# Kernel optimization log

Hardware: AMD Instinct MI355X
Metric: run time of the kernel (lower is better)

Reference implementation:

```python
import jax, jax.numpy as jnp
import numpy as np

NUM_EMBEDDINGS = 1024
EMBEDDING_DIM = 256
COMMITMENT_COST = 0.25
EMA_DECAY = 0.99
EPSILON = 1e-10


def setup_inputs() -> dict:
    key = jax.random.key(0)
    k1, k2, k3 = jax.random.split(key, 3)
    z_e = jax.random.normal(k1, (32, EMBEDDING_DIM, 32, 32), dtype=jnp.float32)
    embedding = jax.random.normal(k2, (NUM_EMBEDDINGS, EMBEDDING_DIM), dtype=jnp.float32)
    ema_cluster_size = jnp.zeros((NUM_EMBEDDINGS,), dtype=jnp.float32)
    ema_w = jax.random.normal(k3, (NUM_EMBEDDINGS, EMBEDDING_DIM), dtype=jnp.float32)
    return {"z_e": z_e, "embedding": embedding,
            "ema_cluster_size": ema_cluster_size, "ema_w": ema_w}


def reference(z_e, embedding, ema_cluster_size, ema_w):
    B, C, H, W = z_e.shape
    K = embedding.shape[0]
    # [B,C,H,W] -> [B,H,W,C] -> [N,C]
    z_bhwc = jnp.transpose(z_e, (0, 2, 3, 1))
    z_flat = z_bhwc.reshape(-1, C)
    N = z_flat.shape[0]

    # squared-L2 distances: ||z||^2 + ||e||^2 - 2 z e^T  -> [N, K]
    distances = (jnp.sum(z_flat * z_flat, axis=1, keepdims=True)
                 + jnp.sum(embedding * embedding, axis=1)
                 - 2.0 * z_flat @ embedding.T)
    indices = jnp.argmin(distances, axis=1)  # [N]

    quantized = embedding[indices].reshape(z_bhwc.shape)  # [B,H,W,C]

    # EMA codebook update (training path); segment_sum replaces one-hot matmul
    counts = jax.ops.segment_sum(jnp.ones((N,), dtype=z_flat.dtype), indices,
                                 num_segments=K)
    new_cluster_size = ema_cluster_size * EMA_DECAY + (1.0 - EMA_DECAY) * counts
    dw = jax.ops.segment_sum(z_flat, indices, num_segments=K)  # [K, C]
    new_ema_w = ema_w * EMA_DECAY + (1.0 - EMA_DECAY) * dw
    n = jnp.sum(new_cluster_size)
    cluster_size = (new_cluster_size + EPSILON) / (n + K * EPSILON) * n
    new_embedding = new_ema_w / cluster_size[:, None]

    loss = COMMITMENT_COST * jnp.mean(
        (jax.lax.stop_gradient(quantized) - z_bhwc) ** 2)
    # straight-through estimator
    q_st = z_bhwc + jax.lax.stop_gradient(quantized - z_bhwc)

    avg_probs = counts / N
    perplexity = jnp.exp(-jnp.sum(avg_probs * jnp.log(avg_probs + 1e-10)))

    q_out = jnp.transpose(q_st, (0, 3, 1, 2))  # [B,C,H,W]
    token_map = indices.reshape(B, H, W)
    return (q_out, loss, perplexity, token_map,
            new_cluster_size, new_ema_w, new_embedding)
```

## Files before the change

### kernel.cpp

```cpp
#include <hip/hip_runtime.h>

#define C_DIM   256
#define HWN     1024
#define N_TOT   32768
#define NELEM   8388608
#define CHW     (C_DIM*HWN)
#define BIGF    3.4e38f
#define FLAG_CAP 8192
#define MARGIN  0.02f

typedef __attribute__((ext_vector_type(8)))  short bf16x8;
typedef __attribute__((ext_vector_type(16))) float f32x16;


__device__ inline unsigned short bf16_rne(float x) {
    unsigned int u = __float_as_uint(x);
    unsigned int r = (u + 0x7FFF + ((u >> 16) & 1)) >> 16;
    return (unsigned short)r;
}
__device__ inline float bf16_to_f(unsigned short h) {
    return __uint_as_float(((unsigned int)h) << 16);
}

__global__ __launch_bounds__(256)
void vq_eprep(const float* __restrict__ e, unsigned short* __restrict__ ebt) {
    const int t = threadIdx.x;
    const int ct = blockIdx.x;
    const int cg = blockIdx.y;
    const int u = t >> 5;
    const int row = t & 31;
    const float* src = e + (size_t)(ct*32 + row)*C_DIM + cg*64 + u*8;
    const float4 v0 = *(const float4*)(src);
    const float4 v1 = *(const float4*)(src + 4);
    const float xs[8] = {v0.x,v0.y,v0.z,v0.w,v1.x,v1.y,v1.z,v1.w};
    __align__(16) unsigned short hi[8], lo[8];
    #pragma unroll
    for (int j = 0; j < 8; j++) {
        hi[j] = bf16_rne(xs[j]);
        lo[j] = bf16_rne(xs[j] - bf16_to_f(hi[j]));
    }
    const int cs = cg*4 + (u >> 1);
    const int lpos = (u & 1)*32 + row;
    unsigned short* dhi = ebt + ((size_t)(ct*2 + 0)*16 + cs)*512 + lpos*8;
    unsigned short* dlo = ebt + ((size_t)(ct*2 + 1)*16 + cs)*512 + lpos*8;
    *(uint4*)dhi = *(const uint4*)hi;
    *(uint4*)dlo = *(const uint4*)lo;
}

__global__ void vq_enorm(const float* __restrict__ e, float* __restrict__ enorm) {
    const int t = threadIdx.x;
    const int w = t >> 6;
    const int lane = t & 63;
    const int k = blockIdx.x * 4 + w;
    const float4 v = *(const float4*)(e + (size_t)k * C_DIM + lane * 4);
    float s = fmaf(v.x, v.x, fmaf(v.y, v.y, fmaf(v.z, v.z, v.w * v.w)));
    #pragma unroll
    for (int off = 32; off > 0; off >>= 1) s += __shfl_down(s, off, 64);
    if (lane == 0) enorm[k] = s;
}

__global__ __launch_bounds__(256)
void vq_zprep(const float* __restrict__ z, unsigned short* __restrict__ zbt) {
    const int t = threadIdx.x;
    const int rt = blockIdx.x;
    const int cg = blockIdx.y;
    const int u = t >> 5;
    const int row = t & 31;
    const int n = rt*32 + row;
    const int b = n >> 10, p = n & 1023;
    const float* zb = z + (size_t)b*CHW + p;
    const int c0 = cg*64 + u*8;
    float xs[8];
    #pragma unroll
    for (int j = 0; j < 8; j++) xs[j] = zb[(size_t)(c0 + j)*HWN];
    __align__(16) unsigned short hi[8], lo[8];
    #pragma unroll
    for (int j = 0; j < 8; j++) {
        hi[j] = bf16_rne(xs[j]);
        lo[j] = bf16_rne(xs[j] - bf16_to_f(hi[j]));
    }
    const int cs = cg*4 + (u >> 1);
    const int lpos = (u & 1)*32 + row;
    unsigned short* base = zbt + (size_t)rt*16384;
    *(uint4*)(base + (0*16 + cs)*512 + lpos*8) = *(const uint4*)hi;
    *(uint4*)(base + (16   + cs)*512 + lpos*8) = *(const uint4*)lo;
}

__global__ __launch_bounds__(256, 2)
void vq_argmin_mfma(const unsigned short* __restrict__ zbt,
                    const unsigned short* __restrict__ ebt,
                    const float* __restrict__ enorm,
                    int* __restrict__ idx_arr, int* __restrict__ counts_i,
                    float* __restrict__ tokmap,
                    int* __restrict__ flag_cnt, int* __restrict__ flags) {
    __shared__ float redd[64][2];
    __shared__ float reds[64][2];
    __shared__ int   redi[64][2];

    const int t = threadIdx.x;
    const int lane = t & 63;
    const int w = t >> 6;
    const int rg = w >> 1;
    const int cg = w & 1;
    const int col = lane & 31;
    const int h = lane >> 5;
    const int n0 = blockIdx.x * 64;
    const int rt = (n0 >> 5) + rg;

    bf16x8 Ahi[16], Alo[16];
    const unsigned short* abase = zbt + (size_t)rt * 16384;
    #pragma unroll
    for (int cs = 0; cs < 16; cs++) {
        Ahi[cs] = *(const bf16x8*)(abase + (0*16 + cs)*512 + lane*8);
        Alo[cs] = *(const bf16x8*)(abase + (16   + cs)*512 + lane*8);
    }

    float bestd[16], secondd[16];
    int   besti[16];
    #pragma unroll
    for (int r = 0; r < 16; r++) { bestd[r] = BIGF; secondd[r] = BIGF; besti[r] = 0x7fffffff; }

    for (int kc = 0; kc < 16; kc++) {
        f32x16 acc = {0,0,0,0,0,0,0,0,0,0,0,0,0,0,0,0};
        const unsigned short* bh_base = ebt + ((size_t)((kc*2 + cg)*2 + 0)*16)*512 + lane*8;
        const unsigned short* bl_base = bh_base + (size_t)16*512;
        #pragma unroll
        for (int cs = 0; cs < 16; cs++) {
            const bf16x8 bh = *(const bf16x8*)(bh_base + (size_t)cs*512);
            const bf16x8 bl = *(const bf16x8*)(bl_base + (size_t)cs*512);
            acc = __builtin_amdgcn_mfma_f32_32x32x16_bf16(Ahi[cs], bh, acc, 0, 0, 0);
            acc = __builtin_amdgcn_mfma_f32_32x32x16_bf16(Ahi[cs], bl, acc, 0, 0, 0);
            acc = __builtin_amdgcn_mfma_f32_32x32x16_bf16(Alo[cs], bh, acc, 0, 0, 0);
        }
        const int code = kc*64 + cg*32 + col;
        const float en = enorm[code];
        #pragma unroll
        for (int r = 0; r < 16; r++) {
            const float d = fmaf(-2.0f, acc[r], en);
            if (d < bestd[r]) { secondd[r] = bestd[r]; bestd[r] = d; besti[r] = code; }
            else if (d < secondd[r]) secondd[r] = d;
        }
    }

    #pragma unroll
    for (int m = 1; m < 32; m <<= 1) {
        #pragma unroll
        for (int r = 0; r < 16; r++) {
            const float od = __shfl_xor(bestd[r],   m, 64);
            const int   oi = __shfl_xor(besti[r],   m, 64);
            const float os = __shfl_xor(secondd[r], m, 64);
            const bool take = (od < bestd[r]) || (od == bestd[r] && oi < besti[r]);
            const float ns = take ? fminf(bestd[r], os) : fminf(secondd[r], od);
            if (take) { bestd[r] = od; besti[r] = oi; }
            secondd[r] = ns;
        }
    }
    __syncthreads();
    if (col == 0) {
        #pragma unroll
        for (int r = 0; r < 16; r++) {
            const int row = (r & 3) + 8*(r >> 2) + 4*h;
            redd[rg*32 + row][cg] = bestd[r];
            redi[rg*32 + row][cg] = besti[r];
            reds[rg*32 + row][cg] = secondd[r];
        }
    }
    __syncthreads();
    if (t < 64) {
        const float d0 = redd[t][0], d1 = redd[t][1];
        const int   i0 = redi[t][0], i1 = redi[t][1];
        const float s0 = reds[t][0], s1 = reds[t][1];
        const bool take = (d1 < d0) || (d1 == d0 && i1 < i0);
        const float bd = take ? d1 : d0;
        const int   bi = take ? i1 : i0;
        const float sd = take ? fminf(d0, s1) : fminf(s0, d1);
        const int n = n0 + t;
        idx_arr[n] = bi;
        tokmap[n] = (float)bi;
        atomicAdd(&counts_i[bi], 1);
        if (sd - bd < MARGIN) {
            const int pos = atomicAdd(flag_cnt, 1);
            if (pos < FLAG_CAP) flags[pos] = n;
        }
    }
}

__global__ __launch_bounds__(256)
void vq_fix(const float* __restrict__ z, const float* __restrict__ e,
            const float* __restrict__ enorm,
            const int* __restrict__ flag_cnt, const int* __restrict__ flags,
            int* __restrict__ idx_arr, int* __restrict__ counts_i,
            float* __restrict__ tokmap) {
    __shared__ float zrow[256];
    __shared__ float rd[256];
    __shared__ int   ri[256];
    const int t = threadIdx.x;
    int cnt = *flag_cnt;
    if (cnt > FLAG_CAP) cnt = FLAG_CAP;
    for (int fi = blockIdx.x; fi < cnt; fi += (int)gridDim.x) {
        const int n = flags[fi];
        const int b = n >> 10, p = n & 1023;
        __syncthreads();
        zrow[t] = z[(size_t)b*CHW + (size_t)t*HWN + p];
        __syncthreads();
        float bd = BIGF; int bi = 0;
        for (int q = 0; q < 4; q++) {
            const int k = t*4 + q;
            const float* er = e + (size_t)k*C_DIM;
            float acc = 0.0f;
            for (int c = 0; c < C_DIM; c += 4) {
                const float4 ev = *(const float4*)(er + c);
                acc = fmaf(ev.x, zrow[c],   acc);
                acc = fmaf(ev.y, zrow[c+1], acc);
                acc = fmaf(ev.z, zrow[c+2], acc);
                acc = fmaf(ev.w, zrow[c+3], acc);
            }
            const float d = fmaf(-2.0f, acc, enorm[k]);
            if (d < bd) { bd = d; bi = k; }
        }
        rd[t] = bd; ri[t] = bi;
        __syncthreads();
        for (int s = 128; s > 0; s >>= 1) {
            if (t < s) {
                const float d2 = rd[t+s]; const int i2 = ri[t+s];
                if (d2 < rd[t] || (d2 == rd[t] && i2 < ri[t])) { rd[t] = d2; ri[t] = i2; }
            }
            __syncthreads();
        }
        if (t == 0) {
            const int old = idx_arr[n];
            if (ri[0] != old) {
                idx_arr[n] = ri[0];
                tokmap[n] = (float)ri[0];
                atomicAdd(&counts_i[old], -1);
                atomicAdd(&counts_i[ri[0]], 1);
            }
        }
        __syncthreads();
    }
}

__global__ void vq_scan_small(const int* __restrict__ counts_i,
                              const float* __restrict__ ema_cs,
                              float* __restrict__ out_perp,
                              float* __restrict__ out_ncs,
                              float* __restrict__ csize,
                              int* __restrict__ base, int* __restrict__ offs) {
    __shared__ float sf[1024];
    __shared__ int si[1024];
    const int t = threadIdx.x;
    const int ci = counts_i[t];
    const float cnt = (float)ci;
    const float ncs = ema_cs[t] * 0.99f + 0.01f * cnt;
    out_ncs[t] = ncs;

    sf[t] = ncs;
    __syncthreads();
    for (int s = 512; s > 0; s >>= 1) { if (t < s) sf[t] += sf[t + s]; __syncthreads(); }
    const float n_total = sf[0];
    __syncthreads();

    csize[t] = (ncs + 1e-10f) / (n_total + 1024.0f * 1e-10f) * n_total;

    const float pr = cnt * (1.0f / 32768.0f);
    sf[t] = pr * logf(pr + 1e-10f);
    __syncthreads();
    for (int s = 512; s > 0; s >>= 1) { if (t < s) sf[t] += sf[t + s]; __syncthreads(); }
    if (t == 0) out_perp[0] = expf(-sf[0]);

    si[t] = ci;
    __syncthreads();
    for (int d = 1; d < 1024; d <<= 1) {
        const int x = si[t];
        const int y = (t >= d) ? si[t - d] : 0;
        __syncthreads();
        si[t] = x + y;
        __syncthreads();
    }
    const int excl = si[t] - ci;
    base[t] = excl;
    offs[t] = excl;
}

__global__ __launch_bounds__(256)
void vq_scatter(const int* __restrict__ idx_arr, int* __restrict__ offs,
                int* __restrict__ order) {
    const int n = blockIdx.x * 256 + threadIdx.x;
    const int idx = idx_arr[n];
    const int pos = atomicAdd(&offs[idx], 1);
    order[pos] = n;
}

__global__ __launch_bounds__(256)
void vq_dw(const unsigned short* __restrict__ zbt, const int* __restrict__ order,
           const int* __restrict__ base, const int* __restrict__ counts_i,
           float* __restrict__ dw) {
    __shared__ int sord[1024];
    __shared__ float red[4][256];
    const int k = blockIdx.x;
    const int t = threadIdx.x;
    const int w = t >> 6;
    const int l = t & 63;
    const int plane = l >> 5;
    const int cs = (l >> 1) & 15;
    const int hh = l & 1;
    const int start = base[k];
    const int cnt = counts_i[k];
    const size_t loff = (size_t)(plane*16 + cs)*512 + hh*256;

    float acc[8] = {0,0,0,0,0,0,0,0};

    for (int s0 = 0; s0 < cnt; s0 += 1024) {
        const int m = min(1024, cnt - s0);
        __syncthreads();
        for (int i = t; i < m; i += 256) sord[i] = order[start + s0 + i];
        __syncthreads();
        const int mm = m & ~31;
        for (int g0 = w*8; g0 < mm; g0 += 32) {
            uint4 v[8];
            #pragma unroll
            for (int r = 0; r < 8; r++) {
                const int n = sord[g0 + r];
                const int rt = n >> 5, row = n & 31;
                v[r] = *(const uint4*)(zbt + (size_t)rt*16384 + loff + row*8);
            }
            #pragma unroll
            for (int r = 0; r < 8; r++) {
                const unsigned short* u = (const unsigned short*)&v[r];
                #pragma unroll
                for (int j = 0; j < 8; j++) acc[j] += bf16_to_f(u[j]);
            }
        }
        for (int i = mm + w; i < m; i += 4) {
            const int n = sord[i];
            const int rt = n >> 5, row = n & 31;
            const uint4 v = *(const uint4*)(zbt + (size_t)rt*16384 + loff + row*8);
            const unsigned short* u = (const unsigned short*)&v;
            #pragma unroll
            for (int j = 0; j < 8; j++) acc[j] += bf16_to_f(u[j]);
        }
    }

    #pragma unroll
    for (int j = 0; j < 8; j++) acc[j] += __shfl_xor(acc[j], 32, 64);
    if (l < 32) {
        #pragma unroll
        for (int j = 0; j < 8; j++) red[w][cs*16 + hh*8 + j] = acc[j];
    }
    __syncthreads();
    dw[(size_t)k*C_DIM + t] = red[0][t] + red[1][t] + red[2][t] + red[3][t];
}

__global__ __launch_bounds__(256)
void vq_combine(const float* __restrict__ z, const float* __restrict__ e,
                const int* __restrict__ idx_arr,
                float* __restrict__ loss_acc,
                float* __restrict__ qout) {
    const int t = threadIdx.x;
    const int n = blockIdx.x * 256 + t;
    const int csplit = blockIdx.y;
    const int b = n >> 10, p = n & 1023;
    const int idx = idx_arr[n];

    const float* zrow = z + (size_t)b*CHW + p;
    float* qrow = qout + (size_t)b*CHW + p;
    const float* erow = e + (size_t)idx*C_DIM;

    float lsum = 0.0f;
    for (int cc = 0; cc < 64; cc += 16) {
        const int cb = csplit*64 + cc;
        float ev[16];
        #pragma unroll
        for (int q4 = 0; q4 < 4; q4++) {
            const float4 v = *(const float4*)(erow + cb + q4*4);
            ev[q4*4+0] = v.x; ev[q4*4+1] = v.y; ev[q4*4+2] = v.z; ev[q4*4+3] = v.w;
        }
        #pragma unroll
        for (int j = 0; j < 16; j++) {
            const float zv = zrow[(size_t)(cb + j) * HWN];
            qrow[(size_t)(cb + j) * HWN] = ev[j];
            const float df = ev[j] - zv;
            lsum = fmaf(df, df, lsum);
        }
    }
    #pragma unroll
    for (int off = 32; off > 0; off >>= 1) lsum += __shfl_down(lsum, off, 64);
    __shared__ float ls[4];
    if ((t & 63) == 0) ls[t >> 6] = lsum;
    __syncthreads();
    if (t == 0) atomicAdd(loss_acc, ls[0] + ls[1] + ls[2] + ls[3]);
}

__global__ __launch_bounds__(256)
void vq_finalize_big(const float* __restrict__ ema_w, const float* __restrict__ dw,
                     const float* __restrict__ csize, const float* __restrict__ loss_acc,
                     float* __restrict__ out_ema_w, float* __restrict__ out_emb,
                     float* __restrict__ out_loss) {
    const int i4 = blockIdx.x * 256 + threadIdx.x;
    const int k = i4 >> 6;
    const float4 w = ((const float4*)ema_w)[i4];
    const float4 d = ((const float4*)dw)[i4];
    float4 nw;
    nw.x = fmaf(w.x, 0.99f, 0.01f * d.x);
    nw.y = fmaf(w.y, 0.99f, 0.01f * d.y);
    nw.z = fmaf(w.z, 0.99f, 0.01f * d.z);
    nw.w = fmaf(w.w, 0.99f, 0.01f * d.w);
    ((float4*)out_ema_w)[i4] = nw;
    const float cs = csize[k];
    float4 ne;
    ne.x = nw.x / cs; ne.y = nw.y / cs; ne.z = nw.z / cs; ne.w = nw.w / cs;
    ((float4*)out_emb)[i4] = ne;
    if (i4 == 0) out_loss[0] = 0.25f * loss_acc[0] * (1.0f / (float)NELEM);
}

extern "C" void kernel_launch(void* const* d_in, const int* in_sizes, int n_in,
                              void* d_out, int out_size, void* d_ws, size_t ws_size,
                              hipStream_t stream) {
    const float* z      = (const float*)d_in[0];
    const float* e      = (const float*)d_in[1];
    const float* ema_cs = (const float*)d_in[2];
    const float* ema_w  = (const float*)d_in[3];
    float* out = (float*)d_out;
    float* ws  = (float*)d_ws;

    int*   idx_arr  = (int*)ws;
    int*   flag_cnt = (int*)(ws + 32768);
    int*   counts_i = (int*)(ws + 32769);
    float* loss_acc = ws + 33793;
    int*   flags    = (int*)(ws + 33794);
    float* enorm    = ws + 41986;
    float* csize    = ws + 43010;
    int*   base     = (int*)(ws + 44034);
    int*   offs     = (int*)(ws + 45058);
    int*   order    = (int*)(ws + 46082);
    unsigned short* ebt = (unsigned short*)(ws + 78852);

    unsigned short* zbt = (unsigned short*)out;
    float* dw = out + 8684546;
    float* tokmap = out + 8388610;

    hipMemsetAsync(ws + 32768, 0, 4104, stream);

    vq_eprep<<<dim3(32, 4), 256, 0, stream>>>(e, ebt);
    vq_enorm<<<256, 256, 0, stream>>>(e, enorm);
    vq_zprep<<<dim3(1024, 4), 256, 0, stream>>>(z, zbt);
    vq_argmin_mfma<<<512, 256, 0, stream>>>(zbt, ebt, enorm, idx_arr, counts_i,
                                            tokmap, flag_cnt, flags);
    vq_fix<<<64, 256, 0, stream>>>(z, e, enorm, flag_cnt, flags, idx_arr, counts_i,
                                   tokmap);
    vq_scan_small<<<1, 1024, 0, stream>>>(counts_i, ema_cs,
                                          out + 8388609, out + 8421378, csize, base, offs);
    vq_scatter<<<128, 256, 0, stream>>>(idx_arr, offs, order);
    vq_dw<<<1024, 256, 0, stream>>>(zbt, order, base, counts_i, dw);
    vq_combine<<<dim3(128, 4), 256, 0, stream>>>(z, e, idx_arr, loss_acc, out);
    vq_finalize_big<<<256, 256, 0, stream>>>(ema_w, dw, csize, loss_acc,
                                             out + 8422402, out + 8684546,
                                             out + 8388608);
}
```

Baseline: 396.0 us.

## Stage codebook tiles in LDS and split the K reduction across waves

The argmin kernel now cooperatively loads each 32-code slab of the bf16 codebook into shared memory, register-prefetching the next slab while computing the current one. Before, every wave streamed its B fragments straight from global memory. The wave pairs now split the channel dimension in half instead of splitting codes, which halves the A-fragment registers per wave. Partial MFMA accumulators are exchanged through LDS to form full dot products, and the final cross-wave argmin reduction is replaced by a per-wave direct write. The cost is two block barriers per 32-code step and twice as many outer iterations.

```diff
diff --git a/kernel.cpp b/kernel.cpp
--- a/kernel.cpp
+++ b/kernel.cpp
@@ -93,94 +93,107 @@
                     int* __restrict__ idx_arr, int* __restrict__ counts_i,
                     float* __restrict__ tokmap,
                     int* __restrict__ flag_cnt, int* __restrict__ flags) {
-    __shared__ float redd[64][2];
-    __shared__ float reds[64][2];
-    __shared__ int   redi[64][2];
+    __shared__ __align__(16) unsigned short Bslab[16384];
+    __shared__ float xbuf[2][2][8][64];
 
     const int t = threadIdx.x;
     const int lane = t & 63;
     const int w = t >> 6;
     const int rg = w >> 1;
-    const int cg = w & 1;
+    const int p  = w & 1;
     const int col = lane & 31;
     const int h = lane >> 5;
     const int n0 = blockIdx.x * 64;
     const int rt = (n0 >> 5) + rg;
 
-    bf16x8 Ahi[16], Alo[16];
+    bf16x8 Ahi[8], Alo[8];
     const unsigned short* abase = zbt + (size_t)rt * 16384;
     #pragma unroll
-    for (int cs = 0; cs < 16; cs++) {
-        Ahi[cs] = *(const bf16x8*)(abase + (0*16 + cs)*512 + lane*8);
-        Alo[cs] = *(const bf16x8*)(abase + (16   + cs)*512 + lane*8);
-    }
-
-    float bestd[16], secondd[16];
-    int   besti[16];
-    #pragma unroll
-    for (int r = 0; r < 16; r++) { bestd[r] = BIGF; secondd[r] = BIGF; besti[r] = 0x7fffffff; }
-
-    for (int kc = 0; kc < 16; kc++) {
+    for (int i = 0; i < 8; i++) {
+        Ahi[i] = *(const bf16x8*)(abase + (0*16 + p*8 + i)*512 + lane*8);
+        Alo[i] = *(const bf16x8*)(abase + (16   + p*8 + i)*512 + lane*8);
+    }
+
+    float bestd[8], secondd[8];
+    int   besti[8];
+    #pragma unroll
+    for (int j = 0; j < 8; j++) { bestd[j] = BIGF; secondd[j] = BIGF; besti[j] = 0x7fffffff; }
+
+    uint4 st[8];
+    {
+        const uint4* src = (const uint4*)ebt;
+        #pragma unroll
+        for (int i = 0; i < 8; i++) st[i] = src[i*256 + t];
+        #pragma unroll
+        for (int i = 0; i < 8; i++) ((uint4*)Bslab)[i*256 + t] = st[i];
+    }
+    __syncthreads();
+
+    for (int kc = 0; kc < 32; kc++) {
+        if (kc < 31) {
+            const uint4* src = (const uint4*)(ebt + (size_t)(kc + 1)*16384);
+            #pragma unroll
+            for (int i = 0; i < 8; i++) st[i] = src[i*256 + t];
+        }
         f32x16 acc = {0,0,0,0,0,0,0,0,0,0,0,0,0,0,0,0};
-        const unsigned short* bh_base = ebt + ((size_t)((kc*2 + cg)*2 + 0)*16)*512 + lane*8;
-        const unsigned short* bl_base = bh_base + (size_t)16*512;
-        #pragma unroll
-        for (int cs = 0; cs < 16; cs++) {
-            const bf16x8 bh = *(const bf16x8*)(bh_base + (size_t)cs*512);
-            const bf16x8 bl = *(const bf16x8*)(bl_base + (size_t)cs*512);
-            acc = __builtin_amdgcn_mfma_f32_32x32x16_bf16(Ahi[cs], bh, acc, 0, 0, 0);
-            acc = __builtin_amdgcn_mfma_f32_32x32x16_bf16(Ahi[cs], bl, acc, 0, 0, 0);
-            acc = __builtin_amdgcn_mfma_f32_32x32x16_bf16(Alo[cs], bh, acc, 0, 0, 0);
-        }
-        const int code = kc*64 + cg*32 + col;
-        const float en = enorm[code];
-        #pragma unroll
-        for (int r = 0; r < 16; r++) {
-            const float d = fmaf(-2.0f, acc[r], en);
-            if (d < bestd[r]) { secondd[r] = bestd[r]; bestd[r] = d; besti[r] = code; }
-            else if (d < secondd[r]) secondd[r] = d;
-        }
+        #pragma unroll
+        for (int i = 0; i < 8; i++) {
+            const bf16x8 bh = *(const bf16x8*)(Bslab + (0*16 + p*8 + i)*512 + lane*8);
+            const bf16x8 bl = *(const bf16x8*)(Bslab + (16   + p*8 + i)*512 + lane*8);
+            acc = __builtin_amdgcn_mfma_f32_32x32x16_bf16(Ahi[i], bh, acc, 0, 0, 0);
+            acc = __builtin_amdgcn_mfma_f32_32x32x16_bf16(Ahi[i], bl, acc, 0, 0, 0);
+            acc = __builtin_amdgcn_mfma_f32_32x32x16_bf16(Alo[i], bh, acc, 0, 0, 0);
+        }
+        if (p == 0) {
+            #pragma unroll
+            for (int j = 0; j < 8; j++) xbuf[rg][1][j][lane] = acc[8 + j];
+        } else {
+            #pragma unroll
+            for (int j = 0; j < 8; j++) xbuf[rg][0][j][lane] = acc[j];
+        }
+        __syncthreads();
+        const float en = enorm[kc*32 + col];
+        const int code = kc*32 + col;
+        #pragma unroll
+        for (int j = 0; j < 8; j++) {
+            const float mine = (p == 0) ? acc[j] : acc[8 + j];
+            const float s = mine + xbuf[rg][p][j][lane];
+            const float d = fmaf(-2.0f, s, en);
+            if (d < bestd[j]) { secondd[j] = bestd[j]; bestd[j] = d; besti[j] = code; }
+            else if (d < secondd[j]) secondd[j] = d;
+        }
+        if (kc < 31) {
+            #pragma unroll
+            for (int i = 0; i < 8; i++) ((uint4*)Bslab)[i*256 + t] = st[i];
+        }
+        __syncthreads();
     }
 
     #pragma unroll
     for (int m = 1; m < 32; m <<= 1) {
         #pragma unroll
-        for (int r = 0; r < 16; r++) {
-            const float od = __shfl_xor(bestd[r],   m, 64);
-            const int   oi = __shfl_xor(besti[r],   m, 64);
-            const float os = __shfl_xor(secondd[r], m, 64);
-            const bool take = (od < bestd[r]) || (od == bestd[r] && oi < besti[r]);
-            const float ns = take ? fminf(bestd[r], os) : fminf(secondd[r], od);
-            if (take) { bestd[r] = od; besti[r] = oi; }
-            secondd[r] = ns;
-        }
-    }
-    __syncthreads();
+        for (int j = 0; j < 8; j++) {
+            const float od = __shfl_xor(bestd[j],   m, 64);
+            const int   oi = __shfl_xor(besti[j],   m, 64);
+            const float os = __shfl_xor(secondd[j], m, 64);
+            const bool take = (od < bestd[j]) || (od == bestd[j] && oi < besti[j]);
+            const float ns = take ? fminf(bestd[j], os) : fminf(secondd[j], od);
+            if (take) { bestd[j] = od; besti[j] = oi; }
+            secondd[j] = ns;
+        }
+    }
     if (col == 0) {
         #pragma unroll
-        for (int r = 0; r < 16; r++) {
-            const int row = (r & 3) + 8*(r >> 2) + 4*h;
-            redd[rg*32 + row][cg] = bestd[r];
-            redi[rg*32 + row][cg] = besti[r];
-            reds[rg*32 + row][cg] = secondd[r];
-        }
-    }
-    __syncthreads();
-    if (t < 64) {
-        const float d0 = redd[t][0], d1 = redd[t][1];
-        const int   i0 = redi[t][0], i1 = redi[t][1];
-        const float s0 = reds[t][0], s1 = reds[t][1];
-        const bool take = (d1 < d0) || (d1 == d0 && i1 < i0);
-        const float bd = take ? d1 : d0;
-        const int   bi = take ? i1 : i0;
-        const float sd = take ? fminf(d0, s1) : fminf(s0, d1);
-        const int n = n0 + t;
-        idx_arr[n] = bi;
-        tokmap[n] = (float)bi;
-        atomicAdd(&counts_i[bi], 1);
-        if (sd - bd < MARGIN) {
-            const int pos = atomicAdd(flag_cnt, 1);
-            if (pos < FLAG_CAP) flags[pos] = n;
+        for (int j = 0; j < 8; j++) {
+            const int row = p*16 + (j & 3) + 8*(j >> 2) + 4*h;
+            const int n = n0 + rg*32 + row;
+            idx_arr[n] = besti[j];
+            tokmap[n] = (float)besti[j];
+            atomicAdd(&counts_i[besti[j]], 1);
+            if (secondd[j] - bestd[j] < MARGIN) {
+                const int pos = atomicAdd(flag_cnt, 1);
+                if (pos < FLAG_CAP) flags[pos] = n;
+            }
         }
     }
 }
```

Result: slower. 500.5 us (+26.4%).

## Compute commitment loss from z norms and min distances, stage A tile in LDS

Applied to the files above, without the earlier changes.

The commitment loss is rebuilt algebraically as the sum of ||z||^2, accumulated in zprep, plus the sum of the minimum distances from the argmin kernel. This lets the combine kernel become a pure quantized-output writer that no longer re-reads z. The argmin kernel now stages the z tile in LDS instead of holding it in registers. It splits the three MFMA chains into independent accumulators and replaces second-best tracking with a near-tie flag bitmask. The tie margin is tightened tenfold and the fix kernel grid is doubled. The smaller margin and the algebraic loss add some risk to index and loss accuracy.

```diff
diff --git a/kernel.cpp b/kernel.cpp
--- a/kernel.cpp
+++ b/kernel.cpp
@@ -7,7 +7,7 @@
 #define CHW     (C_DIM*HWN)
 #define BIGF    3.4e38f
 #define FLAG_CAP 8192
-#define MARGIN  0.02f
+#define MARGIN  0.002f
 
 typedef __attribute__((ext_vector_type(8)))  short bf16x8;
 typedef __attribute__((ext_vector_type(16))) float f32x16;
@@ -60,7 +60,8 @@
 }
 
 __global__ __launch_bounds__(256)
-void vq_zprep(const float* __restrict__ z, unsigned short* __restrict__ zbt) {
+void vq_zprep(const float* __restrict__ z, unsigned short* __restrict__ zbt,
+              float* __restrict__ loss_acc) {
     const int t = threadIdx.x;
     const int rt = blockIdx.x;
     const int cg = blockIdx.y;
@@ -74,16 +75,25 @@
     #pragma unroll
     for (int j = 0; j < 8; j++) xs[j] = zb[(size_t)(c0 + j)*HWN];
     __align__(16) unsigned short hi[8], lo[8];
+    float zn = 0.0f;
     #pragma unroll
     for (int j = 0; j < 8; j++) {
         hi[j] = bf16_rne(xs[j]);
         lo[j] = bf16_rne(xs[j] - bf16_to_f(hi[j]));
+        zn = fmaf(xs[j], xs[j], zn);
     }
     const int cs = cg*4 + (u >> 1);
     const int lpos = (u & 1)*32 + row;
     unsigned short* base = zbt + (size_t)rt*16384;
     *(uint4*)(base + (0*16 + cs)*512 + lpos*8) = *(const uint4*)hi;
     *(uint4*)(base + (16   + cs)*512 + lpos*8) = *(const uint4*)lo;
+
+    #pragma unroll
+    for (int off = 32; off > 0; off >>= 1) zn += __shfl_down(zn, off, 64);
+    __shared__ float ls[4];
+    if ((t & 63) == 0) ls[t >> 6] = zn;
+    __syncthreads();
+    if (t == 0) atomicAdd(loss_acc, ls[0] + ls[1] + ls[2] + ls[3]);
 }
 
 __global__ __launch_bounds__(256, 2)
@@ -91,11 +101,12 @@
                     const unsigned short* __restrict__ ebt,
                     const float* __restrict__ enorm,
                     int* __restrict__ idx_arr, int* __restrict__ counts_i,
-                    float* __restrict__ tokmap,
+                    float* __restrict__ tokmap, float* __restrict__ loss_acc,
                     int* __restrict__ flag_cnt, int* __restrict__ flags) {
+    __shared__ __align__(16) unsigned short Aslab[32768];
     __shared__ float redd[64][2];
-    __shared__ float reds[64][2];
     __shared__ int   redi[64][2];
+    __shared__ int   redf[64][2];
 
     const int t = threadIdx.x;
     const int lane = t & 63;
@@ -105,55 +116,63 @@
     const int col = lane & 31;
     const int h = lane >> 5;
     const int n0 = blockIdx.x * 64;
-    const int rt = (n0 >> 5) + rg;
-
-    bf16x8 Ahi[16], Alo[16];
-    const unsigned short* abase = zbt + (size_t)rt * 16384;
-    #pragma unroll
-    for (int cs = 0; cs < 16; cs++) {
-        Ahi[cs] = *(const bf16x8*)(abase + (0*16 + cs)*512 + lane*8);
-        Alo[cs] = *(const bf16x8*)(abase + (16   + cs)*512 + lane*8);
-    }
-
-    float bestd[16], secondd[16];
+
+    {
+        const uint4* src = (const uint4*)(zbt + (size_t)(blockIdx.x*2)*16384);
+        uint4* dst = (uint4*)Aslab;
+        #pragma unroll
+        for (int i = 0; i < 16; i++) dst[i*256 + t] = src[i*256 + t];
+    }
+    __syncthreads();
+
+    float bestd[16];
     int   besti[16];
-    #pragma unroll
-    for (int r = 0; r < 16; r++) { bestd[r] = BIGF; secondd[r] = BIGF; besti[r] = 0x7fffffff; }
+    unsigned fl = 0;
+    #pragma unroll
+    for (int r = 0; r < 16; r++) { bestd[r] = BIGF; besti[r] = 0x7fffffff; }
+
+    const unsigned short* asl = Aslab + rg*16384;
 
     for (int kc = 0; kc < 16; kc++) {
-        f32x16 acc = {0,0,0,0,0,0,0,0,0,0,0,0,0,0,0,0};
+        f32x16 ahh = {0,0,0,0,0,0,0,0,0,0,0,0,0,0,0,0};
+        f32x16 ahl = {0,0,0,0,0,0,0,0,0,0,0,0,0,0,0,0};
+        f32x16 alh = {0,0,0,0,0,0,0,0,0,0,0,0,0,0,0,0};
         const unsigned short* bh_base = ebt + ((size_t)((kc*2 + cg)*2 + 0)*16)*512 + lane*8;
         const unsigned short* bl_base = bh_base + (size_t)16*512;
         #pragma unroll
         for (int cs = 0; cs < 16; cs++) {
+            const bf16x8 Ah = *(const bf16x8*)(asl + (0*16 + cs)*512 + lane*8);
+            const bf16x8 Al = *(const bf16x8*)(asl + (16   + cs)*512 + lane*8);
             const bf16x8 bh = *(const bf16x8*)(bh_base + (size_t)cs*512);
             const bf16x8 bl = *(const bf16x8*)(bl_base + (size_t)cs*512);
-            acc = __builtin_amdgcn_mfma_f32_32x32x16_bf16(Ahi[cs], bh, acc, 0, 0, 0);
-            acc = __builtin_amdgcn_mfma_f32_32x32x16_bf16(Ahi[cs], bl, acc, 0, 0, 0);
-            acc = __builtin_amdgcn_mfma_f32_32x32x16_bf16(Alo[cs], bh, acc, 0, 0, 0);
+            ahh = __builtin_amdgcn_mfma_f32_32x32x16_bf16(Ah, bh, ahh, 0, 0, 0);
+            ahl = __builtin_amdgcn_mfma_f32_32x32x16_bf16(Ah, bl, ahl, 0, 0, 0);
+            alh = __builtin_amdgcn_mfma_f32_32x32x16_bf16(Al, bh, alh, 0, 0, 0);
         }
         const int code = kc*64 + cg*32 + col;
         const float en = enorm[code];
         #pragma unroll
         for (int r = 0; r < 16; r++) {
-            const float d = fmaf(-2.0f, acc[r], en);
-            if (d < bestd[r]) { secondd[r] = bestd[r]; bestd[r] = d; besti[r] = code; }
-            else if (d < secondd[r]) secondd[r] = d;
+            const float s = ahh[r] + ahl[r] + alh[r];
+            const float d = fmaf(-2.0f, s, en);
+            if (fabsf(d - bestd[r]) < MARGIN) fl |= (1u << r);
+            if (d < bestd[r]) { bestd[r] = d; besti[r] = code; }
         }
     }
 
     #pragma unroll
     for (int m = 1; m < 32; m <<= 1) {
+        const unsigned of = (unsigned)__shfl_xor((int)fl, m, 64);
+        unsigned nf = fl | of;
         #pragma unroll
         for (int r = 0; r < 16; r++) {
-            const float od = __shfl_xor(bestd[r],   m, 64);
-            const int   oi = __shfl_xor(besti[r],   m, 64);
-            const float os = __shfl_xor(secondd[r], m, 64);
+            const float od = __shfl_xor(bestd[r], m, 64);
+            const int   oi = __shfl_xor(besti[r], m, 64);
+            if (fabsf(od - bestd[r]) < MARGIN) nf |= (1u << r);
             const bool take = (od < bestd[r]) || (od == bestd[r] && oi < besti[r]);
-            const float ns = take ? fminf(bestd[r], os) : fminf(secondd[r], od);
             if (take) { bestd[r] = od; besti[r] = oi; }
-            secondd[r] = ns;
-        }
+        }
+        fl = nf;
     }
     __syncthreads();
     if (col == 0) {
@@ -162,26 +181,32 @@
             const int row = (r & 3) + 8*(r >> 2) + 4*h;
             redd[rg*32 + row][cg] = bestd[r];
             redi[rg*32 + row][cg] = besti[r];
-            reds[rg*32 + row][cg] = secondd[r];
-        }
-    }
-    __syncthreads();
+            redf[rg*32 + row][cg] = (fl >> r) & 1;
+        }
+    }
+    __syncthreads();
+    float lsum = 0.0f;
     if (t < 64) {
         const float d0 = redd[t][0], d1 = redd[t][1];
         const int   i0 = redi[t][0], i1 = redi[t][1];
-        const float s0 = reds[t][0], s1 = reds[t][1];
         const bool take = (d1 < d0) || (d1 == d0 && i1 < i0);
         const float bd = take ? d1 : d0;
         const int   bi = take ? i1 : i0;
-        const float sd = take ? fminf(d0, s1) : fminf(s0, d1);
+        const int   flg = redf[t][0] | redf[t][1] | (fabsf(d0 - d1) < MARGIN ? 1 : 0);
         const int n = n0 + t;
         idx_arr[n] = bi;
         tokmap[n] = (float)bi;
         atomicAdd(&counts_i[bi], 1);
-        if (sd - bd < MARGIN) {
+        if (flg) {
             const int pos = atomicAdd(flag_cnt, 1);
             if (pos < FLAG_CAP) flags[pos] = n;
         }
+        lsum = bd;
+    }
+    if (w == 0) {
+        #pragma unroll
+        for (int off = 32; off > 0; off >>= 1) lsum += __shfl_down(lsum, off, 64);
+        if (t == 0) atomicAdd(loss_acc, lsum);
     }
 }
 
@@ -352,43 +377,26 @@
 }
 
 __global__ __launch_bounds__(256)
-void vq_combine(const float* __restrict__ z, const float* __restrict__ e,
-                const int* __restrict__ idx_arr,
-                float* __restrict__ loss_acc,
-                float* __restrict__ qout) {
+void vq_qwrite(const float* __restrict__ e, const int* __restrict__ idx_arr,
+               float* __restrict__ qout) {
     const int t = threadIdx.x;
     const int n = blockIdx.x * 256 + t;
     const int csplit = blockIdx.y;
     const int b = n >> 10, p = n & 1023;
     const int idx = idx_arr[n];
 
-    const float* zrow = z + (size_t)b*CHW + p;
     float* qrow = qout + (size_t)b*CHW + p;
-    const float* erow = e + (size_t)idx*C_DIM;
-
-    float lsum = 0.0f;
-    for (int cc = 0; cc < 64; cc += 16) {
-        const int cb = csplit*64 + cc;
-        float ev[16];
-        #pragma unroll
-        for (int q4 = 0; q4 < 4; q4++) {
-            const float4 v = *(const float4*)(erow + cb + q4*4);
-            ev[q4*4+0] = v.x; ev[q4*4+1] = v.y; ev[q4*4+2] = v.z; ev[q4*4+3] = v.w;
-        }
-        #pragma unroll
-        for (int j = 0; j < 16; j++) {
-            const float zv = zrow[(size_t)(cb + j) * HWN];
-            qrow[(size_t)(cb + j) * HWN] = ev[j];
-            const float df = ev[j] - zv;
-            lsum = fmaf(df, df, lsum);
-        }
-    }
-    #pragma unroll
-    for (int off = 32; off > 0; off >>= 1) lsum += __shfl_down(lsum, off, 64);
-    __shared__ float ls[4];
-    if ((t & 63) == 0) ls[t >> 6] = lsum;
-    __syncthreads();
-    if (t == 0) atomicAdd(loss_acc, ls[0] + ls[1] + ls[2] + ls[3]);
+    const float* erow = e + (size_t)idx*C_DIM + csplit*64;
+
+    #pragma unroll
+    for (int q4 = 0; q4 < 16; q4++) {
+        const float4 v = *(const float4*)(erow + q4*4);
+        const int cb = csplit*64 + q4*4;
+        qrow[(size_t)(cb + 0)*HWN] = v.x;
+        qrow[(size_t)(cb + 1)*HWN] = v.y;
+        qrow[(size_t)(cb + 2)*HWN] = v.z;
+        qrow[(size_t)(cb + 3)*HWN] = v.w;
+    }
 }
 
 __global__ __launch_bounds__(256)
@@ -443,16 +451,16 @@
 
     vq_eprep<<<dim3(32, 4), 256, 0, stream>>>(e, ebt);
     vq_enorm<<<256, 256, 0, stream>>>(e, enorm);
-    vq_zprep<<<dim3(1024, 4), 256, 0, stream>>>(z, zbt);
+    vq_zprep<<<dim3(1024, 4), 256, 0, stream>>>(z, zbt, loss_acc);
     vq_argmin_mfma<<<512, 256, 0, stream>>>(zbt, ebt, enorm, idx_arr, counts_i,
-                                            tokmap, flag_cnt, flags);
-    vq_fix<<<64, 256, 0, stream>>>(z, e, enorm, flag_cnt, flags, idx_arr, counts_i,
-                                   tokmap);
+                                            tokmap, loss_acc, flag_cnt, flags);
+    vq_fix<<<128, 256, 0, stream>>>(z, e, enorm, flag_cnt, flags, idx_arr, counts_i,
+                                    tokmap);
     vq_scan_small<<<1, 1024, 0, stream>>>(counts_i, ema_cs,
                                           out + 8388609, out + 8421378, csize, base, offs);
     vq_scatter<<<128, 256, 0, stream>>>(idx_arr, offs, order);
     vq_dw<<<1024, 256, 0, stream>>>(zbt, order, base, counts_i, dw);
-    vq_combine<<<dim3(128, 4), 256, 0, stream>>>(z, e, idx_arr, loss_acc, out);
+    vq_qwrite<<<dim3(128, 4), 256, 0, stream>>>(e, idx_arr, out);
     vq_finalize_big<<<256, 256, 0, stream>>>(ema_w, dw, csize, loss_acc,
                                              out + 8422402, out + 8684546,
                                              out + 8388608);
```

New measurement: 633.6 us. 1.6x slower.

## Compute commitment loss from argmin distances and z norms instead of rereading z

Applied to the files above, without the earlier changes.

The commitment loss is now built algebraically. The sum of ||z||^2 is accumulated during z prep, and the winning distance term is added in the argmin kernel. The combine kernel becomes a pure quantized-output writer that no longer reads z, which removes a full pass over the input. The near-tie margin that triggers exact fp32 re-checks is cut tenfold, and the fix kernel gets more blocks. This risks small loss inaccuracy for rows whose index the fix kernel later changes, and possible misassigned near-ties under the tighter margin.

```diff
diff --git a/kernel.cpp b/kernel.cpp
--- a/kernel.cpp
+++ b/kernel.cpp
@@ -7,7 +7,7 @@
 #define CHW     (C_DIM*HWN)
 #define BIGF    3.4e38f
 #define FLAG_CAP 8192
-#define MARGIN  0.02f
+#define MARGIN  0.002f
 
 typedef __attribute__((ext_vector_type(8)))  short bf16x8;
 typedef __attribute__((ext_vector_type(16))) float f32x16;
@@ -60,7 +60,8 @@
 }
 
 __global__ __launch_bounds__(256)
-void vq_zprep(const float* __restrict__ z, unsigned short* __restrict__ zbt) {
+void vq_zprep(const float* __restrict__ z, unsigned short* __restrict__ zbt,
+              float* __restrict__ loss_acc) {
     const int t = threadIdx.x;
     const int rt = blockIdx.x;
     const int cg = blockIdx.y;
@@ -74,16 +75,25 @@
     #pragma unroll
     for (int j = 0; j < 8; j++) xs[j] = zb[(size_t)(c0 + j)*HWN];
     __align__(16) unsigned short hi[8], lo[8];
+    float zn = 0.0f;
     #pragma unroll
     for (int j = 0; j < 8; j++) {
         hi[j] = bf16_rne(xs[j]);
         lo[j] = bf16_rne(xs[j] - bf16_to_f(hi[j]));
+        zn = fmaf(xs[j], xs[j], zn);
     }
     const int cs = cg*4 + (u >> 1);
     const int lpos = (u & 1)*32 + row;
     unsigned short* base = zbt + (size_t)rt*16384;
     *(uint4*)(base + (0*16 + cs)*512 + lpos*8) = *(const uint4*)hi;
     *(uint4*)(base + (16   + cs)*512 + lpos*8) = *(const uint4*)lo;
+
+    #pragma unroll
+    for (int off = 32; off > 0; off >>= 1) zn += __shfl_down(zn, off, 64);
+    __shared__ float ls[4];
+    if ((t & 63) == 0) ls[t >> 6] = zn;
+    __syncthreads();
+    if (t == 0) atomicAdd(loss_acc, ls[0] + ls[1] + ls[2] + ls[3]);
 }
 
 __global__ __launch_bounds__(256, 2)
@@ -91,7 +101,7 @@
                     const unsigned short* __restrict__ ebt,
                     const float* __restrict__ enorm,
                     int* __restrict__ idx_arr, int* __restrict__ counts_i,
-                    float* __restrict__ tokmap,
+                    float* __restrict__ tokmap, float* __restrict__ loss_acc,
                     int* __restrict__ flag_cnt, int* __restrict__ flags) {
     __shared__ float redd[64][2];
     __shared__ float reds[64][2];
@@ -166,6 +176,7 @@
         }
     }
     __syncthreads();
+    float lsum = 0.0f;
     if (t < 64) {
         const float d0 = redd[t][0], d1 = redd[t][1];
         const int   i0 = redi[t][0], i1 = redi[t][1];
@@ -182,6 +193,12 @@
             const int pos = atomicAdd(flag_cnt, 1);
             if (pos < FLAG_CAP) flags[pos] = n;
         }
+        lsum = bd;
+    }
+    if (w == 0) {
+        #pragma unroll
+        for (int off = 32; off > 0; off >>= 1) lsum += __shfl_down(lsum, off, 64);
+        if (t == 0) atomicAdd(loss_acc, lsum);
     }
 }
 
@@ -352,43 +369,26 @@
 }
 
 __global__ __launch_bounds__(256)
-void vq_combine(const float* __restrict__ z, const float* __restrict__ e,
-                const int* __restrict__ idx_arr,
-                float* __restrict__ loss_acc,
-                float* __restrict__ qout) {
+void vq_qwrite(const float* __restrict__ e, const int* __restrict__ idx_arr,
+               float* __restrict__ qout) {
     const int t = threadIdx.x;
     const int n = blockIdx.x * 256 + t;
     const int csplit = blockIdx.y;
     const int b = n >> 10, p = n & 1023;
     const int idx = idx_arr[n];
 
-    const float* zrow = z + (size_t)b*CHW + p;
     float* qrow = qout + (size_t)b*CHW + p;
-    const float* erow = e + (size_t)idx*C_DIM;
-
-    float lsum = 0.0f;
-    for (int cc = 0; cc < 64; cc += 16) {
-        const int cb = csplit*64 + cc;
-        float ev[16];
-        #pragma unroll
-        for (int q4 = 0; q4 < 4; q4++) {
-            const float4 v = *(const float4*)(erow + cb + q4*4);
-            ev[q4*4+0] = v.x; ev[q4*4+1] = v.y; ev[q4*4+2] = v.z; ev[q4*4+3] = v.w;
-        }
-        #pragma unroll
-        for (int j = 0; j < 16; j++) {
-            const float zv = zrow[(size_t)(cb + j) * HWN];
-            qrow[(size_t)(cb + j) * HWN] = ev[j];
-            const float df = ev[j] - zv;
-            lsum = fmaf(df, df, lsum);
-        }
-    }
-    #pragma unroll
-    for (int off = 32; off > 0; off >>= 1) lsum += __shfl_down(lsum, off, 64);
-    __shared__ float ls[4];
-    if ((t & 63) == 0) ls[t >> 6] = lsum;
-    __syncthreads();
-    if (t == 0) atomicAdd(loss_acc, ls[0] + ls[1] + ls[2] + ls[3]);
+    const float* erow = e + (size_t)idx*C_DIM + csplit*64;
+
+    #pragma unroll
+    for (int q4 = 0; q4 < 16; q4++) {
+        const float4 v = *(const float4*)(erow + q4*4);
+        const int cb = csplit*64 + q4*4;
+        qrow[(size_t)(cb + 0)*HWN] = v.x;
+        qrow[(size_t)(cb + 1)*HWN] = v.y;
+        qrow[(size_t)(cb + 2)*HWN] = v.z;
+        qrow[(size_t)(cb + 3)*HWN] = v.w;
+    }
 }
 
 __global__ __launch_bounds__(256)
@@ -443,16 +443,16 @@
 
     vq_eprep<<<dim3(32, 4), 256, 0, stream>>>(e, ebt);
     vq_enorm<<<256, 256, 0, stream>>>(e, enorm);
-    vq_zprep<<<dim3(1024, 4), 256, 0, stream>>>(z, zbt);
+    vq_zprep<<<dim3(1024, 4), 256, 0, stream>>>(z, zbt, loss_acc);
     vq_argmin_mfma<<<512, 256, 0, stream>>>(zbt, ebt, enorm, idx_arr, counts_i,
-                                            tokmap, flag_cnt, flags);
-    vq_fix<<<64, 256, 0, stream>>>(z, e, enorm, flag_cnt, flags, idx_arr, counts_i,
-                                   tokmap);
+                                            tokmap, loss_acc, flag_cnt, flags);
+    vq_fix<<<128, 256, 0, stream>>>(z, e, enorm, flag_cnt, flags, idx_arr, counts_i,
+                                    tokmap);
     vq_scan_small<<<1, 1024, 0, stream>>>(counts_i, ema_cs,
                                           out + 8388609, out + 8421378, csize, base, offs);
     vq_scatter<<<128, 256, 0, stream>>>(idx_arr, offs, order);
     vq_dw<<<1024, 256, 0, stream>>>(zbt, order, base, counts_i, dw);
-    vq_combine<<<dim3(128, 4), 256, 0, stream>>>(z, e, idx_arr, loss_acc, out);
+    vq_qwrite<<<dim3(128, 4), 256, 0, stream>>>(e, idx_arr, out);
     vq_finalize_big<<<256, 256, 0, stream>>>(ema_w, dw, csize, loss_acc,
                                              out + 8422402, out + 8684546,
                                              out + 8388608);
```

New measurement: 439.5 us. +11.0%, slower.
